# Performance work log

Measured on AMD Instinct MI355X. Metric: run time of the kernel, lower is better.

Reference implementation:

```python
import jax, jax.numpy as jnp
import numpy as np

K = 8        # num capsules
DD = 64      # per-capsule dim (delta_d)
D = K * DD   # 512
T = 16384    # num target nodes (segments)
NB = 100000  # num neighbor nodes
E = 131072   # num edges
ROUIT = 3
BETA = 0.5


def seg_softmax(p, seg, num):
    # softmax over entries sharing the same segment id (axis 0)
    m = jax.lax.stop_gradient(jax.ops.segment_max(p, seg, num_segments=num))
    e = jnp.exp(p - m[seg])
    s = jax.ops.segment_sum(e, seg, num_segments=num)
    return e / s[seg]


def l2norm(x):
    # F.normalize along last axis with eps=1e-12
    n = jnp.sqrt(jnp.sum(x * x, axis=-1, keepdims=True))
    return x / jnp.maximum(n, 1e-12)


def setup_inputs() -> dict:
    key = jax.random.key(0)
    ks = jax.random.split(key, 9)
    return {
        "x_nb": jax.random.normal(ks[0], (NB, 512), dtype=jnp.float32),
        "ppr": jax.random.uniform(ks[1], (E,), dtype=jnp.float32),
        "pca_w": jax.random.normal(ks[2], (512, D), dtype=jnp.float32) * 0.02,
        "pca_b": jnp.zeros((D,), dtype=jnp.float32),
        "mlp_w": jax.random.normal(ks[3], (D, 40), dtype=jnp.float32) * 0.02,
        "mlp_b": jnp.zeros((40,), dtype=jnp.float32),
        "row_idx": jnp.sort(jax.random.randint(ks[4], (E,), 0, T, dtype=jnp.int32)),
        "col_idx": jax.random.randint(ks[5], (E,), 0, NB, dtype=jnp.int32),
        "x_idx": jax.random.randint(ks[6], (T,), 0, NB, dtype=jnp.int32),
    }


def reference(x_nb, ppr, pca_w, pca_b, mlp_w, mlp_b, row_idx, col_idx, x_idx):
    # pca projection + relu
    x = jax.nn.relu(x_nb @ pca_w + pca_b)            # (NB, D)
    # segment softmax of ppr over targets
    ppr = seg_softmax(ppr, row_idx, T)               # (E,)
    # is_xNorm: per-capsule l2 normalization
    x = l2norm(x.reshape(-1, K, DD)).reshape(-1, D)
    z = x[col_idx]                                   # (E, D) gathered neighbors
    zk = z.reshape(-1, K, DD)                        # (E, K, DD)
    # init_mtd == 2: ppr-weighted scatter-sum init
    u = jax.ops.segment_sum(z * ppr[:, None], row_idx, num_segments=T)  # (T, D)
    for it in range(ROUIT):
        uk = u[row_idx].reshape(-1, K, DD)           # (E, K, DD)
        p = jnp.einsum('ekd,ekd->ek', uk, zk)        # (E, K) capsule logits
        # attention == 1: segment softmax then blend with ppr
        p = seg_softmax(p, row_idx, T)
        p = BETA * p + (1.0 - BETA) * ppr[:, None]
        # final segment softmax
        p = seg_softmax(p, row_idx, T)
        u = jax.ops.segment_sum(zk * p[:, :, None], row_idx, num_segments=T)  # (T, K, DD)
        if it < ROUIT - 1:
            u = l2norm(u)
        u = u.reshape(T, D)
    out = jax.nn.relu(u)                             # dropout is identity at eval
    logits = out @ mlp_w + mlp_b                     # (T, nclass)
    return jax.nn.log_softmax(logits, axis=1)
```

## Files before the change

kernel.cpp:

```cpp
#include <hip/hip_runtime.h>
#include <cstdint>
#include <cstddef>

#define NB_N 100000
#define E_N  131072
#define T_N  16384
#define D_N  512
#define NCLS 40
#define NTILES 782
#define CAPR 12

typedef unsigned short u16;
typedef unsigned int   u32;
typedef __attribute__((ext_vector_type(8))) short  short8;
typedef __attribute__((ext_vector_type(4))) float  floatx4;

__device__ __forceinline__ u16 f2bf(float f) {
  u32 u = __float_as_uint(f);
  return (u16)((u + 0x7fffu + ((u >> 16) & 1u)) >> 16);
}
__device__ __forceinline__ void unpack8(uint4 z, float* f) {
  f[0] = __uint_as_float(z.x << 16);
  f[1] = __uint_as_float(z.x & 0xffff0000u);
  f[2] = __uint_as_float(z.y << 16);
  f[3] = __uint_as_float(z.y & 0xffff0000u);
  f[4] = __uint_as_float(z.z << 16);
  f[5] = __uint_as_float(z.z & 0xffff0000u);
  f[6] = __uint_as_float(z.w << 16);
  f[7] = __uint_as_float(z.w & 0xffff0000u);
}
__device__ __forceinline__ void gload_lds16(const void* g, void* s) {
  __builtin_amdgcn_global_load_lds(
      (const __attribute__((address_space(1))) unsigned int*)g,
      (__attribute__((address_space(3))) unsigned int*)s, 16, 0, 0);
}
__device__ __forceinline__ u32 cvtpk_bf16(float lo, float hi) {
  u32 r;
  asm("v_cvt_pk_bf16_f32 %0, %1, %2" : "=v"(r) : "v"(lo), "v"(hi));
  return r;
}

__global__ void conv_bt(const float* __restrict__ w, u16* __restrict__ Bt) {
  int i = blockIdx.x * 256 + threadIdx.x;
  int n = i >> 9, k = i & 511;
  Bt[i] = f2bf(w[k * 512 + n]);
}

__global__ void conv_bt2(const float* __restrict__ w, u16* __restrict__ Bt2) {
  int i = blockIdx.x * 256 + threadIdx.x;
  int n = i >> 9, k = i & 511;
  Bt2[i] = (n < NCLS) ? f2bf(w[k * NCLS + n]) : (u16)0;
}

__global__ void build_offs(const int* __restrict__ rowi, int* __restrict__ offs) {
  int e = blockIdx.x * 256 + threadIdx.x;
  if (e >= E_N) return;
  int r  = rowi[e];
  int rp = (e == 0) ? -1 : rowi[e - 1];
  for (int t = rp + 1; t <= r; ++t) offs[t] = e;
  if (e == E_N - 1)
    for (int t = r + 1; t <= T_N; ++t) offs[t] = E_N;
}

__global__ void ppr_sm(const float* __restrict__ ppr, const int* __restrict__ offs,
                       float* __restrict__ pprn) {
  int t = blockIdx.x * 256 + threadIdx.x;
  int s = offs[t], en = offs[t + 1];
  if (s >= en) return;
  float m = -INFINITY;
  for (int e = s; e < en; ++e) m = fmaxf(m, ppr[e]);
  float sum = 0.f;
  for (int e = s; e < en; ++e) sum += expf(ppr[e] - m);
  float inv = 1.f / sum;
  for (int e = s; e < en; ++e) pprn[e] = expf(ppr[e] - m) * inv;
}

__global__ __launch_bounds__(256, 3) void gemm_pca(
    const float* __restrict__ A,
    const u16*   __restrict__ Bt,
    const float* __restrict__ bias,
    u16*         __restrict__ xn) {
  __shared__ u16 SMEM[2 * 128 * 64];
  u16* As = SMEM;
  u16* Bs = SMEM + 128 * 64;
  const int tid  = threadIdx.x;
  const int wid  = tid >> 6, lane = tid & 63;
  const int quad = lane >> 4, l16 = lane & 15;
  const int b  = blockIdx.x;
  const int mt = (b & 7) | ((b >> 5) << 3);
  if (mt >= NTILES) return;
  const int m0 = mt * 128;
  const int n0 = ((b >> 3) & 3) * 128;
  const int wm = (wid >> 1) * 64;
  const int wn = (wid & 1) * 64;
  const int sw = l16 & 7;

  floatx4 acc[4][4];
#pragma unroll
  for (int i = 0; i < 4; ++i)
#pragma unroll
    for (int j = 0; j < 4; ++j) acc[i][j] = (floatx4){0.f, 0.f, 0.f, 0.f};

  for (int k0 = 0; k0 < 512; k0 += 64) {
#pragma unroll
    for (int j = 0; j < 4; ++j) {
      int ci  = j * 256 + wid * 64 + lane;
      int row = ci >> 3;
      int kcs = (lane & 7) ^ ((lane >> 3) & 7);
      gload_lds16(Bt + (size_t)(n0 + row) * 512 + k0 + kcs * 8,
                  &Bs[(size_t)(j * 256 + wid * 64) * 8]);
    }
#pragma unroll
    for (int j = 0; j < 4; ++j) {
      int ci  = j * 256 + tid;
      int row = ci >> 3, kc = ci & 7;
      int gm  = m0 + row;
      float4 v0 = make_float4(0.f, 0.f, 0.f, 0.f);
      float4 v1 = make_float4(0.f, 0.f, 0.f, 0.f);
      if (gm < NB_N) {
        const float* src = A + (size_t)gm * 512 + k0 + kc * 8;
        v0 = *(const float4*)(src);
        v1 = *(const float4*)(src + 4);
      }
      uint4 pk;
      pk.x = cvtpk_bf16(v0.x, v0.y);
      pk.y = cvtpk_bf16(v0.z, v0.w);
      pk.z = cvtpk_bf16(v1.x, v1.y);
      pk.w = cvtpk_bf16(v1.z, v1.w);
      int dc = kc ^ (row & 7);
      *(uint4*)(&As[(size_t)(row * 8 + dc) * 8]) = pk;
    }
    __syncthreads();
#pragma unroll
    for (int kk = 0; kk < 64; kk += 32) {
      short8 af[4], bf[4];
#pragma unroll
      for (int mi = 0; mi < 4; ++mi) {
        int c = (kk >> 3) + quad;
        af[mi] = *(const short8*)(&As[(wm + mi * 16 + l16) * 64 + ((c ^ sw) << 3)]);
      }
#pragma unroll
      for (int ni = 0; ni < 4; ++ni) {
        int c = (kk >> 3) + quad;
        bf[ni] = *(const short8*)(&Bs[(wn + ni * 16 + l16) * 64 + ((c ^ sw) << 3)]);
      }
#pragma unroll
      for (int mi = 0; mi < 4; ++mi)
#pragma unroll
        for (int ni = 0; ni < 4; ++ni)
          acc[mi][ni] = __builtin_amdgcn_mfma_f32_16x16x32_bf16(af[mi], bf[ni],
                                                                acc[mi][ni], 0, 0, 0);
    }
    __syncthreads();
  }

  u16* Os = SMEM;
#pragma unroll
  for (int mi = 0; mi < 4; ++mi) {
#pragma unroll
    for (int r = 0; r < 4; ++r) {
      int lrow = wm + mi * 16 + quad * 4 + r;
      float v[4];
      float ss = 0.f;
#pragma unroll
      for (int ni = 0; ni < 4; ++ni) {
        int n  = n0 + wn + ni * 16 + l16;
        float x = acc[mi][ni][r] + bias[n];
        x = fmaxf(x, 0.f);
        v[ni] = x;
        ss += x * x;
      }
      ss += __shfl_xor(ss, 1);
      ss += __shfl_xor(ss, 2);
      ss += __shfl_xor(ss, 4);
      ss += __shfl_xor(ss, 8);
      float sc = 1.f / fmaxf(sqrtf(ss), 1e-12f);
#pragma unroll
      for (int ni = 0; ni < 4; ++ni)
        Os[lrow * 128 + wn + ni * 16 + l16] = f2bf(v[ni] * sc);
    }
  }
  __syncthreads();
#pragma unroll
  for (int c8 = 0; c8 < 8; ++c8) {
    int idx = c8 * 256 + tid;
    int row = idx >> 4, chk = idx & 15;
    int gm = m0 + row;
    if (gm < NB_N) {
      uint4 val = *(const uint4*)(&Os[row * 128 + chk * 8]);
      *(uint4*)(xn + (size_t)gm * 512 + n0 + chk * 8) = val;
    }
  }
}

__device__ __forceinline__ void matvec16(const float (&g0)[16], const float (&g1)[16],
                                         float w0, float w1, int base,
                                         float& e0, float& e1) {
  e0 = 0.f; e1 = 0.f;
#pragma unroll
  for (int j = 0; j < 8; ++j) {
    float wj = __shfl(w0, base | j);
    e0 += g0[j] * wj;
    e1 += g1[j] * wj;
  }
#pragma unroll
  for (int j = 0; j < 8; ++j) {
    float wj = __shfl(w1, base | j);
    e0 += g0[8 + j] * wj;
    e1 += g1[8 + j] * wj;
  }
}

__device__ __forceinline__ void segsm2(float& d0, float& d1, bool v0, bool v1) {
  float m = fmaxf(v0 ? d0 : -INFINITY, v1 ? d1 : -INFINITY);
  m = fmaxf(m, __shfl_xor(m, 1));
  m = fmaxf(m, __shfl_xor(m, 2));
  m = fmaxf(m, __shfl_xor(m, 4));
  float e0 = v0 ? expf(d0 - m) : 0.f;
  float e1 = v1 ? expf(d1 - m) : 0.f;
  float s = e0 + e1;
  s += __shfl_xor(s, 1);
  s += __shfl_xor(s, 2);
  s += __shfl_xor(s, 4);
  float inv = 1.f / s;
  d0 = e0 * inv;
  d1 = e1 * inv;
}

__global__ __launch_bounds__(128, 4) void fused_all(
    const u16* __restrict__ xn, const int* __restrict__ coli,
    const int* __restrict__ offs, const float* __restrict__ pprn,
    u16* __restrict__ ub) {
  __shared__ __align__(16) float Glds[2][8 * 260];
  const int lane = threadIdx.x & 63;
  const int wv = threadIdx.x >> 6;
  const int t = blockIdx.x * 2 + wv;
  const int s = offs[t], en = offs[t + 1];
  int deg = en - s;
  if (deg > 64) deg = 64;

  int   mycol = (lane < deg) ? coli[s + lane] : 0;
  float myppr = (lane < deg) ? pprn[s + lane] : 0.f;

  float uf[8] = {0.f, 0.f, 0.f, 0.f, 0.f, 0.f, 0.f, 0.f};

  if (deg <= 16) {
    float* G = Glds[wv];
    const int esrc = lane & 15, kq = lane >> 4;
    int ce = __shfl(mycol, esrc);
    const u16* zb = xn + (size_t)ce * 512 + kq * 8;
    floatx4 gram[8];
#pragma unroll
    for (int c = 0; c < 8; ++c) {
      short8 f0 = *(const short8*)(zb + c * 64);
      short8 f1 = *(const short8*)(zb + c * 64 + 32);
      floatx4 gg = (floatx4){0.f, 0.f, 0.f, 0.f};
      gg = __builtin_amdgcn_mfma_f32_16x16x32_bf16(f0, f0, gg, 0, 0, 0);
      gg = __builtin_amdgcn_mfma_f32_16x16x32_bf16(f1, f1, gg, 0, 0, 0);
      gram[c] = gg;
    }
#pragma unroll
    for (int c = 0; c < 8; ++c)
      *(float4*)&G[c * 260 + esrc * 16 + kq * 4] = *(float4*)&gram[c];
    const int cc = lane >> 3, i0 = lane & 7;
    const int base = lane & 56;
    float g0[16], g1[16];
    {
      const float* r0 = &G[cc * 260 + i0 * 16];
      const float* r1 = &G[cc * 260 + (i0 + 8) * 16];
#pragma unroll
      for (int ch = 0; ch < 4; ++ch) {
        float4 a = *(const float4*)(r0 + ch * 4);
        float4 b = *(const float4*)(r1 + ch * 4);
        g0[ch * 4 + 0] = a.x; g0[ch * 4 + 1] = a.y;
        g0[ch * 4 + 2] = a.z; g0[ch * 4 + 3] = a.w;
        g1[ch * 4 + 0] = b.x; g1[ch * 4 + 1] = b.y;
        g1[ch * 4 + 2] = b.z; g1[ch * 4 + 3] = b.w;
      }
    }
    const bool v0 = i0 < deg, v1 = (i0 + 8) < deg;
    float pr0 = __shfl(myppr, i0);
    float pr1 = __shfl(myppr, i0 + 8);

    float d0, d1;
    matvec16(g0, g1, pr0, pr1, base, d0, d1);

    float w0 = 0.f, w1 = 0.f;
#pragma unroll
    for (int it = 0; it < 3; ++it) {
      segsm2(d0, d1, v0, v1);
      d0 = 0.5f * d0 + 0.5f * pr0;
      d1 = 0.5f * d1 + 0.5f * pr1;
      segsm2(d0, d1, v0, v1);
      w0 = d0; w1 = d1;
      if (it < 2) {
        float e0, e1;
        matvec16(g0, g1, w0, w1, base, e0, e1);
        float nv = w0 * e0 + w1 * e1;
        nv += __shfl_xor(nv, 1);
        nv += __shfl_xor(nv, 2);
        nv += __shfl_xor(nv, 4);
        float invn = 1.f / fmaxf(sqrtf(nv), 1e-12f);
        d0 = e0 * invn;
        d1 = e1 * invn;
      }
    }

#pragma unroll
    for (int j = 0; j < 16; ++j) {
      if (j < deg) {
        float wj = __shfl((j < 8) ? w0 : w1, base | (j & 7));
        int cj = __shfl(mycol, j);
        uint4 zz = *(const uint4*)(xn + (size_t)cj * 512 + lane * 8);
        float zf[8];
        unpack8(zz, zf);
#pragma unroll
        for (int q = 0; q < 8; ++q) uf[q] += wj * zf[q];
      }
    }
  } else {
    const int cap = lane >> 3;
    const int slot = lane >> 3;

    uint4 zreg[CAPR];
#pragma unroll
    for (int j = 0; j < CAPR; ++j) {
      if (j < deg) {
        int c = __shfl(mycol, j);
        zreg[j] = *(const uint4*)(xn + (size_t)c * 512 + lane * 8);
      }
    }

#pragma unroll
    for (int j = 0; j < CAPR; ++j) {
      if (j < deg) {
        float w = __shfl(myppr, j);
        float zf[8];
        unpack8(zreg[j], zf);
#pragma unroll
        for (int q = 0; q < 8; ++q) uf[q] += w * zf[q];
      }
    }
    for (int j = CAPR; j < deg; ++j) {
      float w = __shfl(myppr, j);
      int c = __shfl(mycol, j);
      uint4 zz = *(const uint4*)(xn + (size_t)c * 512 + lane * 8);
      float zf[8];
      unpack8(zz, zf);
#pragma unroll
      for (int q = 0; q < 8; ++q) uf[q] += w * zf[q];
    }

    float Preg[8];

    for (int it = 0; it < 3; ++it) {
#pragma unroll
      for (int j = 0; j < CAPR; ++j) {
        if (j < deg) {
          float zf[8];
          unpack8(zreg[j], zf);
          float d = uf[0]*zf[0] + uf[1]*zf[1] + uf[2]*zf[2] + uf[3]*zf[3] +
                    uf[4]*zf[4] + uf[5]*zf[5] + uf[6]*zf[6] + uf[7]*zf[7];
          d += __shfl_xor(d, 1);
          d += __shfl_xor(d, 2);
          d += __shfl_xor(d, 4);
          float dc = __shfl(d, (lane & 7) << 3);
          if (slot == (j & 7)) Preg[j >> 3] = dc;
        }
      }
      for (int j = CAPR; j < deg; ++j) {
        int c = __shfl(mycol, j);
        uint4 zz = *(const uint4*)(xn + (size_t)c * 512 + lane * 8);
        float zf[8];
        unpack8(zz, zf);
        float d = uf[0]*zf[0] + uf[1]*zf[1] + uf[2]*zf[2] + uf[3]*zf[3] +
                  uf[4]*zf[4] + uf[5]*zf[5] + uf[6]*zf[6] + uf[7]*zf[7];
        d += __shfl_xor(d, 1);
        d += __shfl_xor(d, 2);
        d += __shfl_xor(d, 4);
        float dc = __shfl(d, (lane & 7) << 3);
        if (slot == (j & 7)) {
          int hi = j >> 3;
          if      (hi == 1) Preg[1] = dc;
          else if (hi == 2) Preg[2] = dc;
          else if (hi == 3) Preg[3] = dc;
          else if (hi == 4) Preg[4] = dc;
          else if (hi == 5) Preg[5] = dc;
          else if (hi == 6) Preg[6] = dc;
          else if (hi == 7) Preg[7] = dc;
        }
      }

      {
        float m1 = -INFINITY;
#pragma unroll
        for (int i = 0; i < 8; ++i)
          m1 = (slot + 8*i < deg) ? fmaxf(m1, Preg[i]) : m1;
        m1 = fmaxf(m1, __shfl_xor(m1, 8));
        m1 = fmaxf(m1, __shfl_xor(m1, 16));
        m1 = fmaxf(m1, __shfl_xor(m1, 32));
        float s1 = 0.f;
#pragma unroll
        for (int i = 0; i < 8; ++i)
          s1 += (slot + 8*i < deg) ? expf(Preg[i] - m1) : 0.f;
        s1 += __shfl_xor(s1, 8);
        s1 += __shfl_xor(s1, 16);
        s1 += __shfl_xor(s1, 32);
        float inv1 = 1.f / s1;
        float m2 = -INFINITY;
#pragma unroll
        for (int i = 0; i < 8; ++i) {
          int j = slot + 8*i;
          if (j < deg) {
            float pj = __shfl(myppr, j);
            float v = 0.5f * expf(Preg[i] - m1) * inv1 + 0.5f * pj;
            Preg[i] = v;
            m2 = fmaxf(m2, v);
          }
        }
        m2 = fmaxf(m2, __shfl_xor(m2, 8));
        m2 = fmaxf(m2, __shfl_xor(m2, 16));
        m2 = fmaxf(m2, __shfl_xor(m2, 32));
        float s2 = 0.f;
#pragma unroll
        for (int i = 0; i < 8; ++i)
          s2 += (slot + 8*i < deg) ? expf(Preg[i] - m2) : 0.f;
        s2 += __shfl_xor(s2, 8);
        s2 += __shfl_xor(s2, 16);
        s2 += __shfl_xor(s2, 32);
        float inv2 = 1.f / s2;
#pragma unroll
        for (int i = 0; i < 8; ++i)
          if (slot + 8*i < deg) Preg[i] = expf(Preg[i] - m2) * inv2;
      }

      float acc[8] = {0.f, 0.f, 0.f, 0.f, 0.f, 0.f, 0.f, 0.f};
#pragma unroll
      for (int j = 0; j < CAPR; ++j) {
        if (j < deg) {
          float w = __shfl(Preg[j >> 3], ((j & 7) << 3) | cap);
          float zf[8];
          unpack8(zreg[j], zf);
#pragma unroll
          for (int q = 0; q < 8; ++q) acc[q] += w * zf[q];
        }
      }
      for (int j = CAPR; j < deg; ++j) {
        int hi = j >> 3;
        float pr = Preg[1];
        if      (hi == 2) pr = Preg[2];
        else if (hi == 3) pr = Preg[3];
        else if (hi == 4) pr = Preg[4];
        else if (hi == 5) pr = Preg[5];
        else if (hi == 6) pr = Preg[6];
        else if (hi == 7) pr = Preg[7];
        float w = __shfl(pr, ((j & 7) << 3) | cap);
        int c = __shfl(mycol, j);
        uint4 zz = *(const uint4*)(xn + (size_t)c * 512 + lane * 8);
        float zf[8];
        unpack8(zz, zf);
#pragma unroll
        for (int q = 0; q < 8; ++q) acc[q] += w * zf[q];
      }
      if (it < 2) {
        float ss = 0.f;
#pragma unroll
        for (int q = 0; q < 8; ++q) ss += acc[q] * acc[q];
        ss += __shfl_xor(ss, 1);
        ss += __shfl_xor(ss, 2);
        ss += __shfl_xor(ss, 4);
        float sc = 1.f / fmaxf(sqrtf(ss), 1e-12f);
#pragma unroll
        for (int q = 0; q < 8; ++q) acc[q] *= sc;
      }
#pragma unroll
      for (int q = 0; q < 8; ++q) uf[q] = acc[q];
    }
  }

  uint4 pk;
  pk.x = (u32)f2bf(fmaxf(uf[0], 0.f)) | ((u32)f2bf(fmaxf(uf[1], 0.f)) << 16);
  pk.y = (u32)f2bf(fmaxf(uf[2], 0.f)) | ((u32)f2bf(fmaxf(uf[3], 0.f)) << 16);
  pk.z = (u32)f2bf(fmaxf(uf[4], 0.f)) | ((u32)f2bf(fmaxf(uf[5], 0.f)) << 16);
  pk.w = (u32)f2bf(fmaxf(uf[6], 0.f)) | ((u32)f2bf(fmaxf(uf[7], 0.f)) << 16);
  *(uint4*)(ub + (size_t)t * 512 + lane * 8) = pk;
}

__global__ __launch_bounds__(256) void mlp_gemm(
    const u16* __restrict__ ub, const u16* __restrict__ Bt2,
    const float* __restrict__ mb, float* __restrict__ out) {
  const int wid = threadIdx.x >> 6, lane = threadIdx.x & 63;
  const int quad = lane >> 4, l16 = lane & 15;
  const int m0 = blockIdx.x * 64 + wid * 16;

  floatx4 acc[4];
#pragma unroll
  for (int ni = 0; ni < 4; ++ni) acc[ni] = (floatx4){0.f, 0.f, 0.f, 0.f};

#pragma unroll 4
  for (int kk = 0; kk < 512; kk += 32) {
    short8 af = *(const short8*)(ub + (size_t)(m0 + l16) * 512 + kk + quad * 8);
#pragma unroll
    for (int ni = 0; ni < 4; ++ni) {
      short8 bf = *(const short8*)(Bt2 + (size_t)(ni * 16 + l16) * 512 + kk + quad * 8);
      acc[ni] = __builtin_amdgcn_mfma_f32_16x16x32_bf16(af, bf, acc[ni], 0, 0, 0);
    }
  }

#pragma unroll
  for (int r = 0; r < 4; ++r) {
    int t = m0 + quad * 4 + r;
    float v[4];
    float mx = -INFINITY;
#pragma unroll
    for (int ni = 0; ni < 4; ++ni) {
      int c = ni * 16 + l16;
      float lg = (c < NCLS) ? (acc[ni][r] + mb[c]) : -INFINITY;
      v[ni] = lg;
      mx = fmaxf(mx, lg);
    }
    mx = fmaxf(mx, __shfl_xor(mx, 1));
    mx = fmaxf(mx, __shfl_xor(mx, 2));
    mx = fmaxf(mx, __shfl_xor(mx, 4));
    mx = fmaxf(mx, __shfl_xor(mx, 8));
    float se = 0.f;
#pragma unroll
    for (int ni = 0; ni < 4; ++ni) {
      int c = ni * 16 + l16;
      if (c < NCLS) se += expf(v[ni] - mx);
    }
    se += __shfl_xor(se, 1);
    se += __shfl_xor(se, 2);
    se += __shfl_xor(se, 4);
    se += __shfl_xor(se, 8);
    float lse = mx + logf(se);
#pragma unroll
    for (int ni = 0; ni < 4; ++ni) {
      int c = ni * 16 + l16;
      if (c < NCLS) out[(size_t)t * NCLS + c] = v[ni] - lse;
    }
  }
}

extern "C" void kernel_launch(void* const* d_in, const int* in_sizes, int n_in,
                              void* d_out, int out_size, void* d_ws, size_t ws_size,
                              hipStream_t stream) {
  const float* x_nb  = (const float*)d_in[0];
  const float* ppr   = (const float*)d_in[1];
  const float* pca_w = (const float*)d_in[2];
  const float* pca_b = (const float*)d_in[3];
  const float* mlp_w = (const float*)d_in[4];
  const float* mlp_b = (const float*)d_in[5];
  const int* row_idx = (const int*)d_in[6];
  const int* col_idx = (const int*)d_in[7];
  float* out = (float*)d_out;

  char* ws = (char*)d_ws;
  const size_t OFF_BT   = 0;
  const size_t OFF_BT2  = 512 * 1024;
  const size_t OFF_PPRN = 640 * 1024;
  const size_t OFF_OFFS = 1152 * 1024;
  const size_t OFF_XN   = 1280 * 1024;
  const size_t OFF_UB   = OFF_XN + (size_t)NB_N * 512 * 2;
  u16*   Bt   = (u16*)(ws + OFF_BT);
  u16*   Bt2  = (u16*)(ws + OFF_BT2);
  float* pprn = (float*)(ws + OFF_PPRN);
  int*   offs = (int*)(ws + OFF_OFFS);
  u16*   xn   = (u16*)(ws + OFF_XN);
  u16*   ub   = (u16*)(ws + OFF_UB);

  conv_bt<<<1024, 256, 0, stream>>>(pca_w, Bt);
  conv_bt2<<<128, 256, 0, stream>>>(mlp_w, Bt2);
  build_offs<<<512, 256, 0, stream>>>(row_idx, offs);
  ppr_sm<<<64, 256, 0, stream>>>(ppr, offs, pprn);

  gemm_pca<<<98 * 32, 256, 0, stream>>>(x_nb, Bt, pca_b, xn);

  fused_all<<<T_N / 2, 128, 0, stream>>>(xn, col_idx, offs, pprn, ub);

  mlp_gemm<<<256, 256, 0, stream>>>(ub, Bt2, mlp_b, out);
}
```

Before: 515.7 us.

## Double-buffer PCA GEMM with register prefetch of A and async B loads

Restructures the PCA GEMM main loop into a software pipeline. LDS is double-buffered, A tiles are prefetched into registers two stages ahead, and B is loaded asynchronously into the next buffer while MFMAs run on the current one. Explicit waitcnt plus barriers replace the two syncthreads per k-step. In exchange, LDS use doubles and register pressure rises, and occupancy is lowered to 2 blocks per SM; out-of-range rows are now clamped rather than zero-filled.

Result: faster. 473.9 us (-8.1%).

```diff
diff --git a/kernel.cpp b/kernel.cpp
--- a/kernel.cpp
+++ b/kernel.cpp
@@ -75,14 +75,14 @@
   for (int e = s; e < en; ++e) pprn[e] = expf(ppr[e] - m) * inv;
 }
 
-__global__ __launch_bounds__(256, 3) void gemm_pca(
+__global__ __launch_bounds__(256, 2) void gemm_pca(
     const float* __restrict__ A,
     const u16*   __restrict__ Bt,
     const float* __restrict__ bias,
     u16*         __restrict__ xn) {
-  __shared__ u16 SMEM[2 * 128 * 64];
+  __shared__ u16 SMEM[4 * 128 * 64];
   u16* As = SMEM;
-  u16* Bs = SMEM + 128 * 64;
+  u16* Bs = SMEM + 16384;
   const int tid  = threadIdx.x;
   const int wid  = tid >> 6, lane = tid & 63;
   const int quad = lane >> 4, l16 = lane & 15;
@@ -101,48 +101,71 @@
 #pragma unroll
     for (int j = 0; j < 4; ++j) acc[i][j] = (floatx4){0.f, 0.f, 0.f, 0.f};
 
-  for (int k0 = 0; k0 < 512; k0 += 64) {
+  float4 pa0[4], pa1[4];
+
+  auto issueA = [&](int k0) {
+#pragma unroll
+    for (int j = 0; j < 4; ++j) {
+      int ci = j * 256 + tid;
+      int row = ci >> 3, kc = ci & 7;
+      int gm = m0 + row;
+      if (gm > NB_N - 1) gm = NB_N - 1;
+      const float* src = A + (size_t)gm * 512 + k0 + kc * 8;
+      pa0[j] = *(const float4*)(src);
+      pa1[j] = *(const float4*)(src + 4);
+    }
+  };
+  auto writeA = [&](u16* dst) {
+#pragma unroll
+    for (int j = 0; j < 4; ++j) {
+      int ci = j * 256 + tid;
+      int row = ci >> 3, kc = ci & 7;
+      uint4 pk;
+      pk.x = cvtpk_bf16(pa0[j].x, pa0[j].y);
+      pk.y = cvtpk_bf16(pa0[j].z, pa0[j].w);
+      pk.z = cvtpk_bf16(pa1[j].x, pa1[j].y);
+      pk.w = cvtpk_bf16(pa1[j].z, pa1[j].w);
+      int dc = kc ^ (row & 7);
+      *(uint4*)(&dst[(size_t)(row * 8 + dc) * 8]) = pk;
+    }
+  };
+  auto issueB = [&](int k0, u16* dstB) {
 #pragma unroll
     for (int j = 0; j < 4; ++j) {
       int ci  = j * 256 + wid * 64 + lane;
       int row = ci >> 3;
       int kcs = (lane & 7) ^ ((lane >> 3) & 7);
       gload_lds16(Bt + (size_t)(n0 + row) * 512 + k0 + kcs * 8,
-                  &Bs[(size_t)(j * 256 + wid * 64) * 8]);
-    }
-#pragma unroll
-    for (int j = 0; j < 4; ++j) {
-      int ci  = j * 256 + tid;
-      int row = ci >> 3, kc = ci & 7;
-      int gm  = m0 + row;
-      float4 v0 = make_float4(0.f, 0.f, 0.f, 0.f);
-      float4 v1 = make_float4(0.f, 0.f, 0.f, 0.f);
-      if (gm < NB_N) {
-        const float* src = A + (size_t)gm * 512 + k0 + kc * 8;
-        v0 = *(const float4*)(src);
-        v1 = *(const float4*)(src + 4);
-      }
-      uint4 pk;
-      pk.x = cvtpk_bf16(v0.x, v0.y);
-      pk.y = cvtpk_bf16(v0.z, v0.w);
-      pk.z = cvtpk_bf16(v1.x, v1.y);
-      pk.w = cvtpk_bf16(v1.z, v1.w);
-      int dc = kc ^ (row & 7);
-      *(uint4*)(&As[(size_t)(row * 8 + dc) * 8]) = pk;
-    }
-    __syncthreads();
+                  &dstB[(size_t)(j * 256 + wid * 64) * 8]);
+    }
+  };
+
+  issueA(0);
+  issueB(0, Bs);
+  writeA(As);
+  issueA(64);
+  asm volatile("s_waitcnt vmcnt(8) lgkmcnt(0)" ::: "memory");
+  __builtin_amdgcn_s_barrier();
+  __builtin_amdgcn_sched_barrier(0);
+
+#pragma unroll
+  for (int s = 0; s < 8; ++s) {
+    const int cur = s & 1, nxt = cur ^ 1;
+    const u16* Asc = As + cur * 8192;
+    const u16* Bsc = Bs + cur * 8192;
+    if (s + 1 < 8) issueB((s + 1) * 64, Bs + nxt * 8192);
 #pragma unroll
     for (int kk = 0; kk < 64; kk += 32) {
       short8 af[4], bf[4];
 #pragma unroll
       for (int mi = 0; mi < 4; ++mi) {
         int c = (kk >> 3) + quad;
-        af[mi] = *(const short8*)(&As[(wm + mi * 16 + l16) * 64 + ((c ^ sw) << 3)]);
+        af[mi] = *(const short8*)(&Asc[(wm + mi * 16 + l16) * 64 + ((c ^ sw) << 3)]);
       }
 #pragma unroll
       for (int ni = 0; ni < 4; ++ni) {
         int c = (kk >> 3) + quad;
-        bf[ni] = *(const short8*)(&Bs[(wn + ni * 16 + l16) * 64 + ((c ^ sw) << 3)]);
+        bf[ni] = *(const short8*)(&Bsc[(wn + ni * 16 + l16) * 64 + ((c ^ sw) << 3)]);
       }
 #pragma unroll
       for (int mi = 0; mi < 4; ++mi)
@@ -151,8 +174,18 @@
           acc[mi][ni] = __builtin_amdgcn_mfma_f32_16x16x32_bf16(af[mi], bf[ni],
                                                                 acc[mi][ni], 0, 0, 0);
     }
-    __syncthreads();
-  }
+    if (s + 1 < 8) writeA(As + nxt * 8192);
+    if (s + 2 < 8) issueA((s + 2) * 64);
+    if (s + 1 < 8) {
+      if (s + 2 < 8)
+        asm volatile("s_waitcnt vmcnt(8) lgkmcnt(0)" ::: "memory");
+      else
+        asm volatile("s_waitcnt vmcnt(0) lgkmcnt(0)" ::: "memory");
+      __builtin_amdgcn_s_barrier();
+      __builtin_amdgcn_sched_barrier(0);
+    }
+  }
+  __syncthreads();
 
   u16* Os = SMEM;
 #pragma unroll
```

## Load GEMM operands directly from global into registers, dropping LDS staging

Applied to the files above, without the earlier changes.

The PCA GEMM no longer stages A and B tiles through shared memory. Each lane now loads its MFMA fragments straight from global memory, converting fp32 A to bf16 in registers, and the loop over k is unrolled by 4. This removes the LDS writes and reads and the two barriers per k-step. In exchange, A is no longer shared across waves, so each A row is fetched once per wave column, which raises global and L2 traffic. Launch bounds drop to 2 blocks per SM, presumably to free registers for the prefetched loads.

Measured after the change: 671.2 us. +30.2%, slower.

```diff
diff --git a/kernel.cpp b/kernel.cpp
--- a/kernel.cpp
+++ b/kernel.cpp
@@ -28,11 +28,6 @@
   f[5] = __uint_as_float(z.z & 0xffff0000u);
   f[6] = __uint_as_float(z.w << 16);
   f[7] = __uint_as_float(z.w & 0xffff0000u);
-}
-__device__ __forceinline__ void gload_lds16(const void* g, void* s) {
-  __builtin_amdgcn_global_load_lds(
-      (const __attribute__((address_space(1))) unsigned int*)g,
-      (__attribute__((address_space(3))) unsigned int*)s, 16, 0, 0);
 }
 __device__ __forceinline__ u32 cvtpk_bf16(float lo, float hi) {
   u32 r;
@@ -75,14 +70,12 @@
   for (int e = s; e < en; ++e) pprn[e] = expf(ppr[e] - m) * inv;
 }
 
-__global__ __launch_bounds__(256, 3) void gemm_pca(
+__global__ __launch_bounds__(256, 2) void gemm_pca(
     const float* __restrict__ A,
     const u16*   __restrict__ Bt,
     const float* __restrict__ bias,
     u16*         __restrict__ xn) {
-  __shared__ u16 SMEM[2 * 128 * 64];
-  u16* As = SMEM;
-  u16* Bs = SMEM + 128 * 64;
+  __shared__ u16 Os[128 * 128];
   const int tid  = threadIdx.x;
   const int wid  = tid >> 6, lane = tid & 63;
   const int quad = lane >> 4, l16 = lane & 15;
@@ -93,7 +86,18 @@
   const int n0 = ((b >> 3) & 3) * 128;
   const int wm = (wid >> 1) * 64;
   const int wn = (wid & 1) * 64;
-  const int sw = l16 & 7;
+
+  const float* a_base[4];
+  const u16*   b_base[4];
+#pragma unroll
+  for (int mi = 0; mi < 4; ++mi) {
+    int gm = m0 + wm + mi * 16 + l16;
+    if (gm > NB_N - 1) gm = NB_N - 1;
+    a_base[mi] = A + (size_t)gm * 512 + quad * 8;
+  }
+#pragma unroll
+  for (int ni = 0; ni < 4; ++ni)
+    b_base[ni] = Bt + (size_t)(n0 + wn + ni * 16 + l16) * 512 + quad * 8;
 
   floatx4 acc[4][4];
 #pragma unroll
@@ -101,60 +105,32 @@
 #pragma unroll
     for (int j = 0; j < 4; ++j) acc[i][j] = (floatx4){0.f, 0.f, 0.f, 0.f};
 
-  for (int k0 = 0; k0 < 512; k0 += 64) {
-#pragma unroll
-    for (int j = 0; j < 4; ++j) {
-      int ci  = j * 256 + wid * 64 + lane;
-      int row = ci >> 3;
-      int kcs = (lane & 7) ^ ((lane >> 3) & 7);
-      gload_lds16(Bt + (size_t)(n0 + row) * 512 + k0 + kcs * 8,
-                  &Bs[(size_t)(j * 256 + wid * 64) * 8]);
-    }
-#pragma unroll
-    for (int j = 0; j < 4; ++j) {
-      int ci  = j * 256 + tid;
-      int row = ci >> 3, kc = ci & 7;
-      int gm  = m0 + row;
-      float4 v0 = make_float4(0.f, 0.f, 0.f, 0.f);
-      float4 v1 = make_float4(0.f, 0.f, 0.f, 0.f);
-      if (gm < NB_N) {
-        const float* src = A + (size_t)gm * 512 + k0 + kc * 8;
-        v0 = *(const float4*)(src);
-        v1 = *(const float4*)(src + 4);
-      }
+#pragma unroll 4
+  for (int k0 = 0; k0 < 512; k0 += 32) {
+    short8 af[4], bf[4];
+#pragma unroll
+    for (int mi = 0; mi < 4; ++mi) {
+      const float4* ap = (const float4*)(a_base[mi] + k0);
+      float4 v0 = ap[0];
+      float4 v1 = ap[1];
       uint4 pk;
       pk.x = cvtpk_bf16(v0.x, v0.y);
       pk.y = cvtpk_bf16(v0.z, v0.w);
       pk.z = cvtpk_bf16(v1.x, v1.y);
       pk.w = cvtpk_bf16(v1.z, v1.w);
-      int dc = kc ^ (row & 7);
-      *(uint4*)(&As[(size_t)(row * 8 + dc) * 8]) = pk;
-    }
-    __syncthreads();
-#pragma unroll
-    for (int kk = 0; kk < 64; kk += 32) {
-      short8 af[4], bf[4];
-#pragma unroll
-      for (int mi = 0; mi < 4; ++mi) {
-        int c = (kk >> 3) + quad;
-        af[mi] = *(const short8*)(&As[(wm + mi * 16 + l16) * 64 + ((c ^ sw) << 3)]);
-      }
-#pragma unroll
-      for (int ni = 0; ni < 4; ++ni) {
-        int c = (kk >> 3) + quad;
-        bf[ni] = *(const short8*)(&Bs[(wn + ni * 16 + l16) * 64 + ((c ^ sw) << 3)]);
-      }
-#pragma unroll
-      for (int mi = 0; mi < 4; ++mi)
-#pragma unroll
-        for (int ni = 0; ni < 4; ++ni)
-          acc[mi][ni] = __builtin_amdgcn_mfma_f32_16x16x32_bf16(af[mi], bf[ni],
-                                                                acc[mi][ni], 0, 0, 0);
-    }
-    __syncthreads();
-  }
-
-  u16* Os = SMEM;
+      af[mi] = *reinterpret_cast<short8*>(&pk);
+    }
+#pragma unroll
+    for (int ni = 0; ni < 4; ++ni)
+      bf[ni] = *(const short8*)(b_base[ni] + k0);
+#pragma unroll
+    for (int mi = 0; mi < 4; ++mi)
+#pragma unroll
+      for (int ni = 0; ni < 4; ++ni)
+        acc[mi][ni] = __builtin_amdgcn_mfma_f32_16x16x32_bf16(af[mi], bf[ni],
+                                                              acc[mi][ni], 0, 0, 0);
+  }
+
 #pragma unroll
   for (int mi = 0; mi < 4; ++mi) {
 #pragma unroll
```
